# Optimization experiments

Measured on AMD Instinct MI355X. Metric: run time of the kernel, lower is better.

Reference implementation:

```python
import jax, jax.numpy as jnp
import numpy as np

NUM_SPECIAL = 3  # rows 1..NUM_SPECIAL in special table; row 0 is padding (zeros)

def setup_inputs() -> dict:
    key = jax.random.key(0)
    ks = jax.random.split(key, 16)
    T, B, E, H, L, V = 128, 32, 512, 512, 2, 32000
    G = 4 * H
    s = 0.02
    special_emb = jax.random.normal(ks[1], (NUM_SPECIAL + 1, E), jnp.float32) * s
    special_emb = special_emb.at[0].set(0.0)  # padding_idx=0
    return {
        "ids": jax.random.randint(ks[0], (T, B), 0, V),
        "length_countdown": jax.random.uniform(ks[2], (T, B, 1), jnp.float32),
        "word_emb": jax.random.normal(ks[3], (V, E), jnp.float32) * s,
        "special_emb": special_emb,
        "h0": jax.random.normal(ks[4], (L, B, H), jnp.float32) * s,
        "c0": jax.random.normal(ks[5], (L, B, H), jnp.float32) * s,
        "prev_output": jnp.zeros((B, H), jnp.float32),
        "Wih0": jax.random.normal(ks[6], (G, E + H + 1), jnp.float32) * s,
        "Whh0": jax.random.normal(ks[7], (G, H), jnp.float32) * s,
        "bih0": jnp.zeros((G,), jnp.float32),
        "bhh0": jnp.zeros((G,), jnp.float32),
        "Wih1": jax.random.normal(ks[8], (G, H), jnp.float32) * s,
        "Whh1": jax.random.normal(ks[9], (G, H), jnp.float32) * s,
        "bih1": jnp.zeros((G,), jnp.float32),
        "bhh1": jnp.zeros((G,), jnp.float32),
        "Wg": jax.random.normal(ks[10], (V, H), jnp.float32) * s,
        "bg": jnp.zeros((V,), jnp.float32),
    }

def _lstm_cell(x, h, c, Wih, Whh, bih, bhh):
    gates = x @ Wih.T + bih + h @ Whh.T + bhh  # [B, 4H]
    i, f, g, o = jnp.split(gates, 4, axis=-1)  # torch LSTMCell gate order
    c_new = jax.nn.sigmoid(f) * c + jax.nn.sigmoid(i) * jnp.tanh(g)
    h_new = jax.nn.sigmoid(o) * jnp.tanh(c_new)
    return h_new, c_new

def reference(ids, length_countdown, word_emb, special_emb, h0, c0, prev_output,
              Wih0, Whh0, bih0, bhh0, Wih1, Whh1, bih1, bhh1, Wg, bg):
    # embeddings = word_embeddings(ids) + special_embeddings(special_ids(ids))
    sp_ids = jnp.where(ids < NUM_SPECIAL, ids + 1, 0)
    emb = word_emb[ids] + special_emb[sp_ids]                 # [T,B,E]
    rnn_in = jnp.concatenate([emb, length_countdown], axis=2)  # [T,B,E+1]

    Wihs = (Wih0, Wih1); Whhs = (Whh0, Whh1)
    bihs = (bih0, bih1); bhhs = (bhh0, bhh1)
    L = h0.shape[0]

    def step(carry, emb_t):
        out, h, c = carry
        x = jnp.concatenate([emb_t, out], axis=1)  # input feeding
        hs, cs = [], []
        for l in range(L):
            h_l, c_l = _lstm_cell(x, h[l], c[l], Wihs[l], Whhs[l], bihs[l], bhhs[l])
            x = h_l  # dropout=0
            hs.append(h_l); cs.append(c_l)
        out = x
        score = jax.nn.log_softmax(out @ Wg.T + bg, axis=-1)  # generator
        return (out, jnp.stack(hs), jnp.stack(cs)), score

    (out, hT, cT), scores = jax.lax.scan(step, (prev_output, h0, c0), rnn_in)
    return scores, (hT, cT), out
```

## Files before the change

### kernel.cpp

```cpp
#include <hip/hip_runtime.h>
#include <hip/hip_bf16.h>


typedef __attribute__((ext_vector_type(8))) short bf16x8;
typedef __attribute__((ext_vector_type(4))) float f32x4;
typedef __attribute__((ext_vector_type(2))) unsigned long long u64x2;

#define AS1 __attribute__((address_space(1)))
#define AS3 __attribute__((address_space(3)))
#define RLX __ATOMIC_RELAXED
#define AGT __HIP_MEMORY_SCOPE_AGENT
#define NGEN 224

__device__ __forceinline__ unsigned short f2bf(float f) {
  unsigned int u = __builtin_bit_cast(unsigned int, f);
  u += 0x7fffu + ((u >> 16) & 1u);
  return (unsigned short)(u >> 16);
}

__device__ __forceinline__ void gl16(const void* g, void* l) {
  __builtin_amdgcn_global_load_lds((const AS1 unsigned int*)g,
                                   (AS3 unsigned int*)l, 16, 0, 0);
}

__device__ __forceinline__ float sigm(float x) { return 1.0f / (1.0f + __expf(-x)); }

__global__ __launch_bounds__(256, 1) void prep_k(
    const float* __restrict__ Wg,  const float* __restrict__ Wih0,
    const float* __restrict__ Whh0,const float* __restrict__ Wih1,
    const float* __restrict__ Whh1,const float* __restrict__ bih0,
    const float* __restrict__ bhh0,const float* __restrict__ bih1,
    const float* __restrict__ bhh1,const float* __restrict__ h0,
    const float* __restrict__ pout,
    unsigned short* __restrict__ WgBf, unsigned short* __restrict__ W0e,
    unsigned short* __restrict__ Wr0p, unsigned short* __restrict__ Wr1p,
    float* __restrict__ b1p, float* __restrict__ bias0c,
    float* __restrict__ wcd, unsigned short* __restrict__ H0X,
    unsigned short* __restrict__ FOUT, unsigned short* __restrict__ H1I)
{
  const long N0 = 16384000L;
  const long N1 = N0 + 1048576L;
  const long N2 = N1 + 2097152L;
  const long N3 = N2 + 2097152L;
  const long N4 = N3 + 2048L;
  const long N5 = N4 + 2048L;
  const long N6 = N5 + 2048L;
  const long N7 = N6 + 49152L;
  for (long i = blockIdx.x * 256L + threadIdx.x; i < N7; i += 256L * gridDim.x) {
    if (i < N0) {
      WgBf[i] = f2bf(Wg[i]);
    } else if (i < N1) {
      long k = i - N0; int g = (int)(k >> 9); int kk = (int)(k & 511);
      W0e[k] = f2bf(Wih0[g * 1025 + kk]);
    } else if (i < N2) {
      long k = i - N1; int gp = (int)(k >> 10); int kk = (int)(k & 1023);
      int j = gp >> 2, gate = gp & 3; int g = gate * 512 + j;
      float v = (kk < 512) ? Whh0[g * 512 + kk] : Wih0[g * 1025 + 513 + (kk - 512)];
      Wr0p[k] = f2bf(v);
    } else if (i < N3) {
      long k = i - N2; int gp = (int)(k >> 10); int kk = (int)(k & 1023);
      int j = gp >> 2, gate = gp & 3; int g = gate * 512 + j;
      float v = (kk < 512) ? Wih1[g * 512 + kk] : Whh1[g * 512 + (kk - 512)];
      Wr1p[k] = f2bf(v);
    } else if (i < N4) {
      int gp = (int)(i - N3); int j = gp >> 2, gate = gp & 3; int g = gate * 512 + j;
      b1p[gp] = bih1[g] + bhh1[g];
    } else if (i < N5) {
      int g = (int)(i - N4); bias0c[g] = bih0[g] + bhh0[g];
    } else if (i < N6) {
      int g = (int)(i - N5); wcd[g] = Wih0[g * 1025 + 512];
    } else {
      long k = i - N6;
      int sub = (int)(k >> 14);
      int e = (int)(k & 16383);
      int wgx = e >> 9, b = (e >> 4) & 31, jl = e & 15;
      int j = wgx * 16 + jl;
      float v = (sub == 0) ? h0[b * 512 + j]
              : (sub == 1) ? h0[16384 + b * 512 + j]
                           : pout[b * 512 + j];
      unsigned short* dst = (sub == 0) ? H0X : (sub == 1) ? H1I : FOUT;
      dst[e] = f2bf(v);
    }
  }
}

__global__ __launch_bounds__(256, 1) void emb_k(
    const int* __restrict__ ids, const float* __restrict__ wemb,
    const float* __restrict__ semb, unsigned short* __restrict__ ebf)
{
  const int tb = blockIdx.x;
  const int id = ids[tb];
  const int sp = (id < 3) ? (id + 1) : 0;
  const float* wr = wemb + (long)id * 512;
  const float* sr = semb + sp * 512;
  for (int i = threadIdx.x; i < 512; i += 256)
    ebf[tb * 512 + i] = f2bf(wr[i] + sr[i]);
}

__global__ __launch_bounds__(256, 1) void gemm_p0(
    const unsigned short* __restrict__ A,
    const unsigned short* __restrict__ B, int N,
    float* __restrict__ C,
    const float* __restrict__ e0, const float* __restrict__ e1,
    const float* __restrict__ e2)
{
  __shared__ unsigned short sA[4096];
  __shared__ unsigned short sB[4096];
  const int tid = threadIdx.x;
  const int l = tid & 63, w = tid >> 6;
  const int nb = N >> 7;
  const int bid = blockIdx.x;
  const int bm = bid / nb, bn = bid - bm * nb;

  const int u0 = w * 128 + l;
  const int u1 = u0 + 64;
  const int r0 = u0 >> 2, c0 = (u0 & 3) ^ (r0 & 3);
  const int r1 = u1 >> 2, c1 = (u1 & 3) ^ (r1 & 3);
  const unsigned short* ga0 = A + (long)(bm * 128 + r0) * 512 + c0 * 8;
  const unsigned short* ga1 = A + (long)(bm * 128 + r1) * 512 + c1 * 8;
  const unsigned short* gb0 = B + (long)(bn * 128 + r0) * 512 + c0 * 8;
  const unsigned short* gb1 = B + (long)(bn * 128 + r1) * 512 + c1 * 8;
  unsigned short* la0 = sA + (w * 2 + 0) * 512;
  unsigned short* la1 = sA + (w * 2 + 1) * 512;
  unsigned short* lb0 = sB + (w * 2 + 0) * 512;
  unsigned short* lb1 = sB + (w * 2 + 1) * 512;

  const int fr = l & 15, fc = l >> 4;
  const int wm = w >> 1, wn = w & 1;
  int aoff[4], boff[4];
#pragma unroll
  for (int mi = 0; mi < 4; ++mi) {
    int row = wm * 64 + mi * 16 + fr;
    aoff[mi] = row * 64 + ((fc ^ (row & 3)) * 16);
  }
#pragma unroll
  for (int ni = 0; ni < 4; ++ni) {
    int row = wn * 64 + ni * 16 + fr;
    boff[ni] = row * 64 + ((fc ^ (row & 3)) * 16);
  }

  f32x4 acc[4][4];
#pragma unroll
  for (int i = 0; i < 4; ++i)
#pragma unroll
    for (int jq = 0; jq < 4; ++jq) acc[i][jq] = (f32x4){0.f, 0.f, 0.f, 0.f};

  for (int kt = 0; kt < 16; ++kt) {
    __syncthreads();
    gl16(ga0 + kt * 32, la0);
    gl16(ga1 + kt * 32, la1);
    gl16(gb0 + kt * 32, lb0);
    gl16(gb1 + kt * 32, lb1);
    asm volatile("s_waitcnt vmcnt(0)" ::: "memory");
    __syncthreads();
    bf16x8 av[4], bv[4];
#pragma unroll
    for (int mi = 0; mi < 4; ++mi)
      av[mi] = *(const bf16x8*)((const char*)sA + aoff[mi]);
#pragma unroll
    for (int ni = 0; ni < 4; ++ni)
      bv[ni] = *(const bf16x8*)((const char*)sB + boff[ni]);
#pragma unroll
    for (int mi = 0; mi < 4; ++mi)
#pragma unroll
      for (int ni = 0; ni < 4; ++ni)
        acc[mi][ni] = __builtin_amdgcn_mfma_f32_16x16x32_bf16(av[mi], bv[ni], acc[mi][ni], 0, 0, 0);
  }

  const int mbase = bm * 128 + wm * 64;
  const int nbase = bn * 128 + wn * 64;
#pragma unroll
  for (int mi = 0; mi < 4; ++mi)
#pragma unroll
    for (int ni = 0; ni < 4; ++ni) {
      const int col = nbase + ni * 16 + fr;
#pragma unroll
      for (int r = 0; r < 4; ++r) {
        const int row = mbase + mi * 16 + fc * 4 + r;
        const int gp = ((row & 511) << 2) | (row >> 9);
        float v = acc[mi][ni][r] + e0[row] + e2[col] * e1[row];
        C[(long)gp * N + col] = v;
      }
    }
}

__global__ __launch_bounds__(256, 1) void lstm_seq(
    const unsigned short* __restrict__ Wr0p,
    const unsigned short* __restrict__ Wr1p,
    float* __restrict__ P0t, const float* __restrict__ b1p,
    const float* __restrict__ c0in,
    unsigned short* __restrict__ H0X, unsigned short* __restrict__ H1X,
    const unsigned short* __restrict__ FOUT, const unsigned short* __restrict__ H1I,
    unsigned short* __restrict__ outbf, float* __restrict__ outs,
    unsigned int* __restrict__ flagA, unsigned int* __restrict__ flagB,
    unsigned int* __restrict__ flagC,
    const unsigned short* __restrict__ WgBf, const float* __restrict__ bg)
{
  const int tid = threadIdx.x;
  __shared__ char smem[75264] __attribute__((aligned(16)));

  if (blockIdx.x < 32) {
    unsigned short* sx = (unsigned short*)smem;
    float (*sg)[65] = (float(*)[65])(smem + 65536);
    unsigned short (*sh)[16] = (unsigned short(*)[16])(smem + 73856);

    const int wg = blockIdx.x;
    const int l = tid & 63, w = tid >> 6;
    const int fr = l & 15, fc = l >> 4;
    const int b = tid & 31, jl0 = tid >> 5;
    const int sb = l >> 1, sjh = l & 1;

    float c0r[2], c1r[2], h0k[2], h1k[2];
#pragma unroll
    for (int jq = 0; jq < 2; ++jq) {
      c0r[jq] = c0in[b * 512 + wg * 16 + jl0 + jq * 8];
      c1r[jq] = c0in[16384 + b * 512 + wg * 16 + jl0 + jq * 8];
      h0k[jq] = 0.f; h1k[jq] = 0.f;
    }

    float b1v[8];
#pragma unroll
    for (int jq = 0; jq < 2; ++jq)
#pragma unroll
      for (int g = 0; g < 4; ++g)
        b1v[jq * 4 + g] = b1p[(wg * 16 + jl0 + jq * 8) * 4 + g];

    const char* sxb0 = (const char*)sx + fr * 2048;
    const char* sxb1 = (const char*)sx + (16 + fr) * 2048;
    const int xr = (fr & 7) << 4;
    const int wrow = (wg * 64 + w * 16 + fr) * 1024 + fc * 8;

    char* const sxw = (char*)sx + sb * 2048;
    const int sswz = (sb & 7) << 4;

#define STAGE2(srcp, half)                                                    \
  do {                                                                        \
    unsigned long long q0[8], q1[8];                                          \
    _Pragma("unroll")                                                         \
    for (int i = 0; i < 8; ++i) {                                             \
      int u = i * 256 + tid;                                                  \
      q0[i] = __hip_atomic_load((const unsigned long long*)(srcp) + u * 2,    \
                                RLX, AGT);                                    \
      q1[i] = __hip_atomic_load((const unsigned long long*)(srcp) + u * 2 + 1,\
                                RLX, AGT);                                    \
    }                                                                         \
    _Pragma("unroll")                                                         \
    for (int i = 0; i < 8; ++i) {                                             \
      int cb = (half) * 1024 + (i * 4 + w) * 32 + sjh * 16;                   \
      u64x2 v; v.x = q0[i]; v.y = q1[i];                                      \
      *(u64x2*)(sxw + (cb ^ sswz)) = v;                                       \
    }                                                                         \
  } while (0)

#define MFMA_HALF(Wp, k0, a0v, a1v)                                           \
  do {                                                                        \
    _Pragma("unroll")                                                         \
    for (int kt = (k0); kt < (k0) + 16; ++kt) {                               \
      bf16x8 bv = *(const bf16x8*)((Wp) + wrow + kt * 32);                    \
      bf16x8 x0 = *(const bf16x8*)(sxb0 + ((kt * 64 + fc * 16) ^ xr));        \
      bf16x8 x1 = *(const bf16x8*)(sxb1 + ((kt * 64 + fc * 16) ^ xr));        \
      a0v = __builtin_amdgcn_mfma_f32_16x16x32_bf16(x0, bv, a0v, 0, 0, 0);    \
      a1v = __builtin_amdgcn_mfma_f32_16x16x32_bf16(x1, bv, a1v, 0, 0, 0);    \
    }                                                                         \
  } while (0)

#define POLL(flags, tgt)                                                      \
  do {                                                                        \
    const unsigned int* fp = (flags) + ((l & 31) << 5);                       \
    for (;;) {                                                                \
      unsigned int f = __hip_atomic_load(fp, RLX, AGT);                       \
      if (__all((int)(f >= (unsigned int)(tgt)))) break;                      \
      __builtin_amdgcn_s_sleep(1);                                            \
    }                                                                         \
    asm volatile("" ::: "memory");                                            \
  } while (0)

    STAGE2(H0X, 0);
    __syncthreads();
    if (tid == 0)
      __hip_atomic_store(&flagB[wg << 5], 1u, RLX, AGT);

    for (int t = 0; t < 128; ++t) {
      float p0v[8];
#pragma unroll
      for (int jq = 0; jq < 2; ++jq)
#pragma unroll
        for (int g = 0; g < 4; ++g)
          p0v[jq * 4 + g] =
              P0t[(long)((wg * 16 + jl0 + jq * 8) * 4 + g) * 4096 + t * 32 + b];

      f32x4 accA0 = (f32x4){0.f, 0.f, 0.f, 0.f};
      f32x4 accA1 = (f32x4){0.f, 0.f, 0.f, 0.f};
      MFMA_HALF(Wr0p, 0, accA0, accA1);

      POLL(flagB, t + 1);
      if (t == 0) STAGE2(FOUT, 1); else STAGE2(H1X, 1);
      __syncthreads();
      MFMA_HALF(Wr0p, 16, accA0, accA1);
#pragma unroll
      for (int r = 0; r < 4; ++r) {
        sg[fc * 4 + r][w * 16 + fr] = accA0[r];
        sg[16 + fc * 4 + r][w * 16 + fr] = accA1[r];
      }
      __syncthreads();
#pragma unroll
      for (int jq = 0; jq < 2; ++jq) {
        const int jl = jl0 + jq * 8;
        float gi = sg[b][jl * 4 + 0] + p0v[jq * 4 + 0];
        float gf = sg[b][jl * 4 + 1] + p0v[jq * 4 + 1];
        float gg = sg[b][jl * 4 + 2] + p0v[jq * 4 + 2];
        float go = sg[b][jl * 4 + 3] + p0v[jq * 4 + 3];
        float cn = sigm(gf) * c0r[jq] + sigm(gi) * tanhf(gg);
        float hn = sigm(go) * tanhf(cn);
        c0r[jq] = cn; h0k[jq] = hn;
        sh[b][jl] = f2bf(hn);
      }
      __syncthreads();
      if (w == 0) {
        u64x2 v = *(const u64x2*)&sh[sb][sjh * 8];
        unsigned long long* dst =
            (unsigned long long*)(H0X + wg * 512 + sb * 16 + sjh * 8);
        __hip_atomic_store(dst,     v.x, RLX, AGT);
        __hip_atomic_store(dst + 1, v.y, RLX, AGT);
        asm volatile("s_waitcnt vmcnt(0)" ::: "memory");
        if (tid == 0)
          __hip_atomic_store(&flagA[wg << 5], (unsigned int)(t + 1), RLX, AGT);
      }

      f32x4 accB0 = (f32x4){0.f, 0.f, 0.f, 0.f};
      f32x4 accB1 = (f32x4){0.f, 0.f, 0.f, 0.f};
      if (t == 0) {
        STAGE2(H1I, 1);
        __syncthreads();
      }
      MFMA_HALF(Wr1p, 16, accB0, accB1);

      POLL(flagA, t + 1);
      STAGE2(H0X, 0);
      __syncthreads();
      MFMA_HALF(Wr1p, 0, accB0, accB1);
#pragma unroll
      for (int r = 0; r < 4; ++r) {
        sg[fc * 4 + r][w * 16 + fr] = accB0[r];
        sg[16 + fc * 4 + r][w * 16 + fr] = accB1[r];
      }
      __syncthreads();
#pragma unroll
      for (int jq = 0; jq < 2; ++jq) {
        const int jl = jl0 + jq * 8;
        float gi = sg[b][jl * 4 + 0] + b1v[jq * 4 + 0];
        float gf = sg[b][jl * 4 + 1] + b1v[jq * 4 + 1];
        float gg = sg[b][jl * 4 + 2] + b1v[jq * 4 + 2];
        float go = sg[b][jl * 4 + 3] + b1v[jq * 4 + 3];
        float cn = sigm(gf) * c1r[jq] + sigm(gi) * tanhf(gg);
        float hn = sigm(go) * tanhf(cn);
        c1r[jq] = cn; h1k[jq] = hn;
        sh[b][jl] = f2bf(hn);
      }
      __syncthreads();
      if (w == 0) {
        u64x2 v = *(const u64x2*)&sh[sb][sjh * 8];
        unsigned long long* dst =
            (unsigned long long*)(H1X + wg * 512 + sb * 16 + sjh * 8);
        __hip_atomic_store(dst,     v.x, RLX, AGT);
        __hip_atomic_store(dst + 1, v.y, RLX, AGT);
        asm volatile("s_waitcnt vmcnt(0)" ::: "memory");
        if (tid == 0)
          __hip_atomic_store(&flagB[wg << 5], (unsigned int)(t + 2), RLX, AGT);
      } else if (w == 1) {
        const unsigned long long* s = (const unsigned long long*)&sh[sb][sjh * 8];
        unsigned long long* dst =
            (unsigned long long*)(outbf + (t * 32 + sb) * 512 + wg * 16 + sjh * 8);
        __hip_atomic_store(dst,     s[0], RLX, AGT);
        __hip_atomic_store(dst + 1, s[1], RLX, AGT);
        asm volatile("s_waitcnt vmcnt(0)" ::: "memory");
        if (l == 0)
          __hip_atomic_store(&flagC[wg << 5], (unsigned int)(t + 1), RLX, AGT);
      }
    }
#undef STAGE2
#undef MFMA_HALF
#undef POLL

    float* hT = outs + 131072000;
    float* cT = outs + 131072000 + 32768;
    float* oT = outs + 131072000 + 65536;
#pragma unroll
    for (int jq = 0; jq < 2; ++jq) {
      const int j = wg * 16 + jl0 + jq * 8;
      hT[b * 512 + j] = h0k[jq];
      hT[16384 + b * 512 + j] = h1k[jq];
      cT[b * 512 + j] = c0r[jq];
      cT[16384 + b * 512 + j] = c1r[jq];
      oT[b * 512 + j] = h1k[jq];
    }
    return;
  }

  {
    unsigned short* sA = (unsigned short*)smem;
    unsigned short* sB = (unsigned short*)(smem + 8192);
    float (*pmw)[2][2] = (float(*)[2][2])(smem + 16384);

    const int g = (int)blockIdx.x - 32;
    const int l = tid & 63, w = tid >> 6;
    const int fr = l & 15, fc = l >> 4;
    const int wm = w >> 1, wn = w & 1;

    const int u0 = w * 128 + l, u1 = u0 + 64;
    const int r0 = u0 >> 2, c0 = (u0 & 3) ^ (r0 & 3);
    const int r1 = u1 >> 2, c1 = (u1 & 3) ^ (r1 & 3);
    unsigned short* lb0 = sB + (w * 2 + 0) * 512;
    unsigned short* lb1 = sB + (w * 2 + 1) * 512;

    int aoff[4], boff[4];
#pragma unroll
    for (int mi = 0; mi < 4; ++mi) {
      int row = wm * 64 + mi * 16 + fr;
      aoff[mi] = row * 64 + ((fc ^ (row & 3)) * 16);
    }
#pragma unroll
    for (int ni = 0; ni < 4; ++ni) {
      int row = wn * 64 + ni * 16 + fr;
      boff[ni] = row * 64 + ((fc ^ (row & 3)) * 16);
    }

    for (int job = g; job < 8000; job += NGEN) {
      const int bm = job / 250, bn = job - bm * 250;

      if (w == 0) {
        const unsigned int* fp = flagC + ((l & 31) << 5);
        const unsigned int tgt = (unsigned int)(4 * bm + 4);
        for (;;) {
          unsigned int f = __hip_atomic_load(fp, RLX, AGT);
          if (__all((int)(f >= tgt))) break;
          __builtin_amdgcn_s_sleep(16);
        }
        asm volatile("" ::: "memory");
      }
      __syncthreads();

      const unsigned short* Ab0 = outbf + (long)(bm * 128 + r0) * 512 + c0 * 8;
      const unsigned short* Ab1 = outbf + (long)(bm * 128 + r1) * 512 + c1 * 8;
      const unsigned short* gb0 = WgBf + (long)(bn * 128 + r0) * 512 + c0 * 8;
      const unsigned short* gb1 = WgBf + (long)(bn * 128 + r1) * 512 + c1 * 8;

      f32x4 acc[4][4];
#pragma unroll
      for (int i = 0; i < 4; ++i)
#pragma unroll
        for (int jq = 0; jq < 4; ++jq) acc[i][jq] = (f32x4){0.f, 0.f, 0.f, 0.f};

      for (int kt = 0; kt < 16; ++kt) {
        __syncthreads();
        unsigned long long a0x = __hip_atomic_load((const unsigned long long*)(Ab0 + kt * 32),     RLX, AGT);
        unsigned long long a0y = __hip_atomic_load((const unsigned long long*)(Ab0 + kt * 32) + 1, RLX, AGT);
        unsigned long long a1x = __hip_atomic_load((const unsigned long long*)(Ab1 + kt * 32),     RLX, AGT);
        unsigned long long a1y = __hip_atomic_load((const unsigned long long*)(Ab1 + kt * 32) + 1, RLX, AGT);
        gl16(gb0 + kt * 32, lb0);
        gl16(gb1 + kt * 32, lb1);
        { u64x2 va; va.x = a0x; va.y = a0y; *(u64x2*)((char*)sA + u0 * 16) = va; }
        { u64x2 va; va.x = a1x; va.y = a1y; *(u64x2*)((char*)sA + u1 * 16) = va; }
        asm volatile("s_waitcnt vmcnt(0)" ::: "memory");
        __syncthreads();
        bf16x8 av[4], bv[4];
#pragma unroll
        for (int mi = 0; mi < 4; ++mi)
          av[mi] = *(const bf16x8*)((const char*)sA + aoff[mi]);
#pragma unroll
        for (int ni = 0; ni < 4; ++ni)
          bv[ni] = *(const bf16x8*)((const char*)sB + boff[ni]);
#pragma unroll
        for (int mi = 0; mi < 4; ++mi)
#pragma unroll
          for (int ni = 0; ni < 4; ++ni)
            acc[mi][ni] = __builtin_amdgcn_mfma_f32_16x16x32_bf16(av[mi], bv[ni], acc[mi][ni], 0, 0, 0);
      }

      const int mbase = bm * 128 + wm * 64;
      const int nbase = bn * 128 + wn * 64;
      float m2[4][4], s2[4][4];
#pragma unroll
      for (int mi = 0; mi < 4; ++mi)
#pragma unroll
        for (int r = 0; r < 4; ++r) { m2[mi][r] = -3.0e38f; s2[mi][r] = 0.f; }
#pragma unroll
      for (int mi = 0; mi < 4; ++mi)
#pragma unroll
        for (int ni = 0; ni < 4; ++ni) {
          const int col = nbase + ni * 16 + fr;
          const float bgc = bg[col];
#pragma unroll
          for (int r = 0; r < 4; ++r) {
            float v = acc[mi][ni][r] + bgc;
            acc[mi][ni][r] = v;
            outs[(long)(mbase + mi * 16 + fc * 4 + r) * 32000L + col] = v;
            m2[mi][r] = fmaxf(m2[mi][r], v);
          }
        }
#pragma unroll
      for (int mi = 0; mi < 4; ++mi)
#pragma unroll
        for (int r = 0; r < 4; ++r)
#pragma unroll
          for (int s = 1; s < 16; s <<= 1)
            m2[mi][r] = fmaxf(m2[mi][r], __shfl_xor(m2[mi][r], s));
#pragma unroll
      for (int mi = 0; mi < 4; ++mi)
#pragma unroll
        for (int ni = 0; ni < 4; ++ni)
#pragma unroll
          for (int r = 0; r < 4; ++r)
            s2[mi][r] += __expf(acc[mi][ni][r] - m2[mi][r]);
#pragma unroll
      for (int mi = 0; mi < 4; ++mi)
#pragma unroll
        for (int r = 0; r < 4; ++r)
#pragma unroll
          for (int s = 1; s < 16; s <<= 1)
            s2[mi][r] += __shfl_xor(s2[mi][r], s);
      if (fr == 0) {
#pragma unroll
        for (int mi = 0; mi < 4; ++mi)
#pragma unroll
          for (int r = 0; r < 4; ++r) {
            const int rl = wm * 64 + mi * 16 + fc * 4 + r;
            pmw[rl][wn][0] = m2[mi][r];
            pmw[rl][wn][1] = s2[mi][r];
          }
      }
      __syncthreads();
      if (tid < 128) {
        float ma = pmw[tid][0][0], sa = pmw[tid][0][1];
        float mb = pmw[tid][1][0], sb2 = pmw[tid][1][1];
        float M = fmaxf(ma, mb);
        float S = sa * __expf(ma - M) + sb2 * __expf(mb - M);
        int q2 = 2 * (tid * 250 + bn);
        float* p = P0t + ((long)(q2 >> 7)) * 4096 + 128L * bm + (q2 & 127);
        p[0] = M; p[1] = S;
      }
      __syncthreads();
    }
  }
}

__global__ __launch_bounds__(256, 1) void lse_fix(float* __restrict__ sc,
                                                  const float* __restrict__ pmsbase)
{
  const long row = blockIdx.x;
  const int bm = (int)(row >> 7), rl = (int)(row & 127);
  float4* p4 = (float4*)(sc + row * 32000L);
  const int tid = threadIdx.x;
  float m = -3.0e38f, s = 0.0f;
  if (tid < 250) {
    int q2 = 2 * (rl * 250 + tid);
    const float* p = pmsbase + ((long)(q2 >> 7)) * 4096 + 128L * bm + (q2 & 127);
    m = p[0]; s = p[1];
  }
#pragma unroll
  for (int off = 32; off > 0; off >>= 1) {
    float mo = __shfl_down(m, off);
    float so = __shfl_down(s, off);
    float mn = fmaxf(m, mo);
    s = s * __expf(m - mn) + so * __expf(mo - mn);
    m = mn;
  }
  __shared__ float lm[4], ls[4], lse_sh;
  if ((tid & 63) == 0) { lm[tid >> 6] = m; ls[tid >> 6] = s; }
  __syncthreads();
  if (tid == 0) {
    float M = lm[0], S = ls[0];
#pragma unroll
    for (int i = 1; i < 4; ++i) {
      float mn = fmaxf(M, lm[i]);
      S = S * __expf(M - mn) + ls[i] * __expf(lm[i] - mn);
      M = mn;
    }
    lse_sh = M + __logf(S);
  }
  __syncthreads();
  const float lse = lse_sh;
  for (int i = tid; i < 8000; i += 256) {
    float4 v = p4[i];
    v.x -= lse; v.y -= lse; v.z -= lse; v.w -= lse;
    p4[i] = v;
  }
}

extern "C" void kernel_launch(void* const* d_in, const int* in_sizes, int n_in,
                              void* d_out, int out_size, void* d_ws, size_t ws_size,
                              hipStream_t stream) {
  const int*   ids  = (const int*)d_in[0];
  const float* cd   = (const float*)d_in[1];
  const float* wemb = (const float*)d_in[2];
  const float* semb = (const float*)d_in[3];
  const float* h0   = (const float*)d_in[4];
  const float* c0   = (const float*)d_in[5];
  const float* pout = (const float*)d_in[6];
  const float* Wih0 = (const float*)d_in[7];
  const float* Whh0 = (const float*)d_in[8];
  const float* bih0 = (const float*)d_in[9];
  const float* bhh0 = (const float*)d_in[10];
  const float* Wih1 = (const float*)d_in[11];
  const float* Whh1 = (const float*)d_in[12];
  const float* bih1 = (const float*)d_in[13];
  const float* bhh1 = (const float*)d_in[14];
  const float* Wg   = (const float*)d_in[15];
  const float* bg   = (const float*)d_in[16];
  float* out = (float*)d_out;

  char* ws = (char*)d_ws;
  unsigned short* WgBf   = (unsigned short*)(ws);
  unsigned short* W0e    = (unsigned short*)(ws + 32768000);
  unsigned short* Wr0p   = (unsigned short*)(ws + 34865152);
  unsigned short* Wr1p   = (unsigned short*)(ws + 39059456);
  float*          b1p    = (float*)(ws + 43253760);
  float*          bias0c = (float*)(ws + 43261952);
  float*          wcd    = (float*)(ws + 43270144);
  unsigned short* embbf  = (unsigned short*)(ws + 43278336);
  unsigned short* outbf  = (unsigned short*)(ws + 47472640);
  float*          P0t    = (float*)(ws + 51666944);
  unsigned int*   flagA  = (unsigned int*)(ws + 85221376);
  unsigned int*   flagB  = (unsigned int*)(ws + 85225472);
  unsigned short* H0X    = (unsigned short*)(ws + 85229568);
  unsigned short* H1X    = (unsigned short*)(ws + 85262336);
  unsigned short* FOUT   = (unsigned short*)(ws + 85295104);
  unsigned short* H1I    = (unsigned short*)(ws + 85327872);
  unsigned int*   flagC  = (unsigned int*)(ws + 85360640);

  hipMemsetAsync((void*)flagA, 0, 8192, stream);
  hipMemsetAsync((void*)flagC, 0, 4096, stream);

  prep_k<<<8192, 256, 0, stream>>>(Wg, Wih0, Whh0, Wih1, Whh1,
                                   bih0, bhh0, bih1, bhh1, h0, pout,
                                   WgBf, W0e, Wr0p, Wr1p, b1p, bias0c, wcd,
                                   H0X, FOUT, H1I);

  emb_k<<<4096, 256, 0, stream>>>(ids, wemb, semb, embbf);

  gemm_p0<<<512, 256, 0, stream>>>(W0e, embbf, 4096, P0t, bias0c, wcd, cd);

  lstm_seq<<<32 + NGEN, 256, 0, stream>>>(Wr0p, Wr1p, P0t, b1p, c0,
                                          H0X, H1X, FOUT, H1I, outbf, out,
                                          flagA, flagB, flagC, WgBf, bg);

  lse_fix<<<4096, 256, 0, stream>>>(out, P0t);
}
```

Baseline: 1.797 ms.

## Fuse log-softmax normalization into persistent kernel via per-row-block completion counters

Removes the separate lse_fix launch and gives 48 blocks of the persistent LSTM kernel the job of subtracting the log-sum-exp from each score row. Each row block is released once all 250 column tiles for it have signalled through an atomic counter, so the normalization overlaps with the ongoing recurrence and generator GEMM. In exchange, 48 fewer blocks do generator GEMM work (224 to 176), and the stores and loads now go through atomics with explicit waits.

```diff
diff --git a/kernel.cpp b/kernel.cpp
--- a/kernel.cpp
+++ b/kernel.cpp
@@ -10,7 +10,8 @@
 #define AS3 __attribute__((address_space(3)))
 #define RLX __ATOMIC_RELAXED
 #define AGT __HIP_MEMORY_SCOPE_AGENT
-#define NGEN 224
+#define NGEN 176
+#define NSUB 48
 
 __device__ __forceinline__ unsigned short f2bf(float f) {
   unsigned int u = __builtin_bit_cast(unsigned int, f);
@@ -193,7 +194,7 @@
     const unsigned short* __restrict__ FOUT, const unsigned short* __restrict__ H1I,
     unsigned short* __restrict__ outbf, float* __restrict__ outs,
     unsigned int* __restrict__ flagA, unsigned int* __restrict__ flagB,
-    unsigned int* __restrict__ flagC,
+    unsigned int* __restrict__ flagC, unsigned int* __restrict__ cntBM,
     const unsigned short* __restrict__ WgBf, const float* __restrict__ bg)
 {
   const int tid = threadIdx.x;
@@ -397,7 +398,7 @@
     return;
   }
 
-  {
+  if (blockIdx.x < 32 + NGEN) {
     unsigned short* sA = (unsigned short*)smem;
     unsigned short* sB = (unsigned short*)(smem + 8192);
     float (*pmw)[2][2] = (float(*)[2][2])(smem + 16384);
@@ -494,7 +495,8 @@
           for (int r = 0; r < 4; ++r) {
             float v = acc[mi][ni][r] + bgc;
             acc[mi][ni][r] = v;
-            outs[(long)(mbase + mi * 16 + fc * 4 + r) * 32000L + col] = v;
+            __hip_atomic_store(&outs[(long)(mbase + mi * 16 + fc * 4 + r) * 32000L + col],
+                               v, RLX, AGT);
             m2[mi][r] = fmaxf(m2[mi][r], v);
           }
         }
@@ -536,54 +538,82 @@
         float M = fmaxf(ma, mb);
         float S = sa * __expf(ma - M) + sb2 * __expf(mb - M);
         int q2 = 2 * (tid * 250 + bn);
-        float* p = P0t + ((long)(q2 >> 7)) * 4096 + 128L * bm + (q2 & 127);
-        p[0] = M; p[1] = S;
-      }
-      __syncthreads();
-    }
+        unsigned long long* p = (unsigned long long*)
+            (P0t + ((long)(q2 >> 7)) * 4096 + 128L * bm + (q2 & 127));
+        float2 o; o.x = M; o.y = S;
+        __hip_atomic_store(p, __builtin_bit_cast(unsigned long long, o), RLX, AGT);
+      }
+      asm volatile("s_waitcnt vmcnt(0)" ::: "memory");
+      __syncthreads();
+      if (tid == 0)
+        __hip_atomic_fetch_add(&cntBM[bm << 5], 1u, RLX, AGT);
+      __syncthreads();
+    }
+    return;
   }
-}
-
-__global__ __launch_bounds__(256, 1) void lse_fix(float* __restrict__ sc,
-                                                  const float* __restrict__ pmsbase)
-{
-  const long row = blockIdx.x;
-  const int bm = (int)(row >> 7), rl = (int)(row & 127);
-  float4* p4 = (float4*)(sc + row * 32000L);
-  const int tid = threadIdx.x;
-  float m = -3.0e38f, s = 0.0f;
-  if (tid < 250) {
-    int q2 = 2 * (rl * 250 + tid);
-    const float* p = pmsbase + ((long)(q2 >> 7)) * 4096 + 128L * bm + (q2 & 127);
-    m = p[0]; s = p[1];
-  }
-#pragma unroll
-  for (int off = 32; off > 0; off >>= 1) {
-    float mo = __shfl_down(m, off);
-    float so = __shfl_down(s, off);
-    float mn = fmaxf(m, mo);
-    s = s * __expf(m - mn) + so * __expf(mo - mn);
-    m = mn;
-  }
-  __shared__ float lm[4], ls[4], lse_sh;
-  if ((tid & 63) == 0) { lm[tid >> 6] = m; ls[tid >> 6] = s; }
-  __syncthreads();
-  if (tid == 0) {
-    float M = lm[0], S = ls[0];
-#pragma unroll
-    for (int i = 1; i < 4; ++i) {
-      float mn = fmaxf(M, lm[i]);
-      S = S * __expf(M - mn) + ls[i] * __expf(lm[i] - mn);
-      M = mn;
-    }
-    lse_sh = M + __logf(S);
-  }
-  __syncthreads();
-  const float lse = lse_sh;
-  for (int i = tid; i < 8000; i += 256) {
-    float4 v = p4[i];
-    v.x -= lse; v.y -= lse; v.z -= lse; v.w -= lse;
-    p4[i] = v;
+
+  {
+    float* red = (float*)smem;
+    const int s = (int)blockIdx.x - 32 - NGEN;
+
+    for (int row = s; row < 4096; row += NSUB) {
+      const int bm = row >> 7, rl = row & 127;
+      if (tid == 0) {
+        for (;;) {
+          unsigned c = __hip_atomic_load(&cntBM[bm << 5], RLX, AGT);
+          if (c >= 250u) break;
+          __builtin_amdgcn_s_sleep(32);
+        }
+      }
+      __syncthreads();
+      asm volatile("" ::: "memory");
+
+      float m = -3.0e38f, sm = 0.0f;
+      if (tid < 250) {
+        int q2 = 2 * (rl * 250 + tid);
+        const unsigned long long* pp = (const unsigned long long*)
+            (P0t + ((long)(q2 >> 7)) * 4096 + 128L * bm + (q2 & 127));
+        unsigned long long q = __hip_atomic_load(pp, RLX, AGT);
+        float2 f = __builtin_bit_cast(float2, q);
+        m = f.x; sm = f.y;
+      }
+#pragma unroll
+      for (int off = 32; off > 0; off >>= 1) {
+        float mo = __shfl_down(m, off);
+        float so = __shfl_down(sm, off);
+        float mn = fmaxf(m, mo);
+        sm = sm * __expf(m - mn) + so * __expf(mo - mn);
+        m = mn;
+      }
+      if ((tid & 63) == 0) { red[tid >> 6] = m; red[4 + (tid >> 6)] = sm; }
+      __syncthreads();
+      if (tid == 0) {
+        float M = red[0], S = red[4];
+#pragma unroll
+        for (int i = 1; i < 4; ++i) {
+          float mn = fmaxf(M, red[i]);
+          S = S * __expf(M - mn) + red[4 + i] * __expf(red[i] - mn);
+          M = mn;
+        }
+        red[8] = M + __logf(S);
+      }
+      __syncthreads();
+      const float lse = red[8];
+
+      float* pr = outs + (long)row * 32000L;
+#pragma unroll 2
+      for (int i = tid; i < 8000; i += 256) {
+        const unsigned long long* lp = (const unsigned long long*)(pr + i * 4);
+        unsigned long long qa = __hip_atomic_load(lp,     RLX, AGT);
+        unsigned long long qb = __hip_atomic_load(lp + 1, RLX, AGT);
+        float2 fa = __builtin_bit_cast(float2, qa);
+        float2 fb = __builtin_bit_cast(float2, qb);
+        float4 v;
+        v.x = fa.x - lse; v.y = fa.y - lse; v.z = fb.x - lse; v.w = fb.y - lse;
+        *(float4*)(pr + i * 4) = v;
+      }
+      __syncthreads();
+    }
   }
 }
 
@@ -627,9 +657,10 @@
   unsigned short* FOUT   = (unsigned short*)(ws + 85295104);
   unsigned short* H1I    = (unsigned short*)(ws + 85327872);
   unsigned int*   flagC  = (unsigned int*)(ws + 85360640);
+  unsigned int*   cntBM  = (unsigned int*)(ws + 85364736);
 
   hipMemsetAsync((void*)flagA, 0, 8192, stream);
-  hipMemsetAsync((void*)flagC, 0, 4096, stream);
+  hipMemsetAsync((void*)flagC, 0, 8192, stream);
 
   prep_k<<<8192, 256, 0, stream>>>(Wg, Wih0, Whh0, Wih1, Whh1,
                                    bih0, bhh0, bih1, bhh1, h0, pout,
@@ -640,9 +671,8 @@
 
   gemm_p0<<<512, 256, 0, stream>>>(W0e, embbf, 4096, P0t, bias0c, wcd, cd);
 
-  lstm_seq<<<32 + NGEN, 256, 0, stream>>>(Wr0p, Wr1p, P0t, b1p, c0,
-                                          H0X, H1X, FOUT, H1I, outbf, out,
-                                          flagA, flagB, flagC, WgBf, bg);
-
-  lse_fix<<<4096, 256, 0, stream>>>(out, P0t);
+  lstm_seq<<<32 + NGEN + NSUB, 256, 0, stream>>>(Wr0p, Wr1p, P0t, b1p, c0,
+                                                 H0X, H1X, FOUT, H1I, outbf, out,
+                                                 flagA, flagB, flagC, cntBM,
+                                                 WgBf, bg);
 }
```

New measurement: 1.731 ms. -3.7%, faster.
